# Optimization experiments

Hardware: AMD Instinct MI355X
Metric: run time of the kernel (lower is better)

The kernel has to match this reference:

```python
import jax, jax.numpy as jnp
import numpy as np

INPUT_SHIFT = 0.1
K = 3  # extract_image_patches(x, 3) hardcodes 3x3 patches


def extract_image_patches(x, k):
    # x: [B, C, H, W] -> [B, k*k*C, Ho, Wo], patch ordering (kh, kw, C)
    B, C, H, W = x.shape
    Ho, Wo = H - k + 1, W - k + 1
    slices = [x[:, :, i:i + Ho, j:j + Wo] for i in range(k) for j in range(k)]
    return jnp.concatenate(slices, axis=1)


def smooth_max(z, axis):
    # SMorph smooth maximum: sum(z * softmax(z)) along axis
    w = jax.nn.softmax(z, axis=axis)
    return jnp.sum(z * w, axis=axis)


def _branch(logp, kflat):
    # logp: [B, P, Ho, Wo]; kflat: [P, O] -> [B, O, Ho, Wo]
    z = logp[:, :, None] + kflat[None, :, :, None, None]  # [B, P, O, Ho, Wo]
    return jnp.exp(smooth_max(z, axis=1))


def setup_inputs() -> dict:
    key = jax.random.key(0)
    kx, kk1, kk2 = jax.random.split(key, 3)
    B, C, H, W, O = 4, 32, 32, 32, 64
    fan_in = K * K * C
    fan_out = K * K * O
    limit = float(np.sqrt(6.0 / (fan_in + fan_out)))  # xavier_uniform
    x = jax.random.normal(kx, (B, C, H, W), dtype=jnp.float32)
    k1 = jax.random.uniform(kk1, (K, K, C, O), minval=-limit, maxval=limit, dtype=jnp.float32)
    k2 = jax.random.uniform(kk2, (K, K, C, O), minval=-limit, maxval=limit, dtype=jnp.float32)
    bias = jnp.zeros((O,), dtype=jnp.float32)
    return {"x": x, "k1": k1, "k2": k2, "bias": bias}


def reference(x, k1, k2, bias):
    kh, kw, C, O = k1.shape
    k1f = k1.reshape(kh * kw * C, O)
    k2f = k2.reshape(kh * kw * C, O)
    # log of clamped patches for +x and -x
    p1 = jnp.log(jnp.maximum(extract_image_patches(x, K), INPUT_SHIFT))
    p2 = jnp.log(jnp.maximum(extract_image_patches(-x, K), INPUT_SHIFT))
    y11 = _branch(p1, k1f)
    y12 = _branch(p1, k2f)
    y21 = _branch(p2, k1f)
    y22 = _branch(p2, k2f)
    return y11 - y12 - y21 + y22 + bias[None, :, None, None]
```

## Files before the change

kernel.cpp:

```cpp
#include <hip/hip_runtime.h>
#include <math.h>


typedef float  f32x4 __attribute__((ext_vector_type(4)));
typedef short  s16x8 __attribute__((ext_vector_type(8)));

#define BB   4
#define CC   32
#define HH   32
#define WW   32
#define OO   64
#define HO   30
#define WO   30
#define NSP  900
#define KDIM 576

#define T1   131072
#define TB   18432

__device__ __forceinline__ unsigned short f2bf(float f) {
    unsigned u = __float_as_uint(f);
    return (unsigned short)((u + 0x7FFFu + ((u >> 16) & 1u)) >> 16);
}

__global__ __launch_bounds__(256) void smorph_prep(
    const float* __restrict__ x, const float* __restrict__ k1,
    const float* __restrict__ k2, float4* __restrict__ pixs,
    unsigned* __restrict__ pixm, unsigned short* __restrict__ bt)
{
    const int t = blockIdx.x * 256 + threadIdx.x;

    if (t < T1) {
        const int pix = t >> 5, c = t & 31;
        const int b = pix >> 10, h = (pix >> 5) & 31, w = pix & 31;
        float v = x[b*32768 + c*1024 + h*32 + w];
        float mp = fmaxf(v, 0.1f), mn = fmaxf(-v, 0.1f);
        float lp = mp * logf(mp), ln_ = mn * logf(mn);
        pixm[pix*64      + c] = (unsigned)f2bf(mp) | ((unsigned)f2bf(lp)  << 16);
        pixm[pix*64 + 32 + c] = (unsigned)f2bf(mn) | ((unsigned)f2bf(ln_) << 16);
        float s0 = mp, s1 = lp, s2 = mn, s3 = ln_;
#pragma unroll
        for (int m = 16; m >= 1; m >>= 1) {
            s0 += __shfl_xor(s0, m); s1 += __shfl_xor(s1, m);
            s2 += __shfl_xor(s2, m); s3 += __shfl_xor(s3, m);
        }
        if (c == 0) pixs[pix] = make_float4(s0, s1, s2, s3);
    } else if (t < T1 + TB) {
        const int u3 = t - T1;
        const int o = u3 & 63, p = u3 >> 6;
        const float a = k1[u3], b2 = k2[u3];
        const float d1 = expm1f(a),  q1 = a  * expf(a);
        const float d2 = expm1f(b2), q2 = b2 * expf(b2);
        const float vals[4][2] = {{d1, 0.f}, {q1, d1}, {d2, 0.f}, {q2, d2}};
#pragma unroll
        for (int tbl = 0; tbl < 4; ++tbl) {
            const int n = o*4 + tbl;
#pragma unroll
            for (int ks = 0; ks < 2; ++ks) {
                const int k    = 2*p + ks;
                const int st   = k >> 5, k32 = k & 31;
                const int lane = (n & 15) + ((k32 >> 3) << 4);
                bt[((n >> 4)*18 + st)*512 + lane*8 + (k32 & 7)] = f2bf(vals[tbl][ks]);
            }
        }
    }
}

__global__ __launch_bounds__(256, 2) void smorph_gemm(
    const unsigned* __restrict__ pixm, const unsigned short* __restrict__ bt,
    const float4* __restrict__ pixs, const float* __restrict__ bias,
    float* __restrict__ out)
{
    __shared__ float cmb[2][2048];
    __shared__ __align__(16) float epi[2][32*66];

    const int tid = threadIdx.x;
    const int l   = tid & 63;
    const int w   = tid >> 6;
    const int kq  = w >> 1;
    const int nhf = w & 1;
    const int bm  = blockIdx.x >> 1;
    const int nh  = blockIdx.x & 1;
    const int N0  = nh*128 + nhf*64;
    const int ng0 = N0 >> 4;

    const int lr = l & 15;
    const int lg = l >> 4;

    float4 S;
    {
        const int s  = bm*16 + lr;
        const int b  = s / NSP, r = s - b*NSP;
        const int ho = r / WO,  wo = r - WO*(r/WO);
        const float4* P = pixs + (b*1024 + ho*32 + wo);
        float4 a = make_float4(0,0,0,0);
#pragma unroll
        for (int kh = 0; kh < 3; ++kh)
#pragma unroll
            for (int kw = 0; kw < 3; ++kw) {
                float4 v = P[kh*32 + kw];
                a.x += v.x; a.y += v.y; a.z += v.z; a.w += v.w;
            }
        S = a;
    }

    unsigned offA[2];
    {
        const int sign = lr & 1;
#pragma unroll
        for (int mi = 0; mi < 2; ++mi) {
            const int s  = bm*16 + mi*8 + (lr >> 1);
            const int b  = s / NSP, r = s - b*NSP;
            const int ho = r / WO,  wo = r - WO*(r/WO);
            const int pix = b*1024 + ho*32 + wo;
            offA[mi] = (unsigned)(pix*256 + sign*128 + lg*16);
        }
    }

    const char* pa = (const char*)pixm;
    const char* pb = (const char*)bt;

    f32x4 acc[2][4] = {};

#pragma unroll
    for (int s2 = 0; s2 < 9; ++s2) {
        const int step  = s2*2 + kq;
        const int khkw  = step >> 1;
        const int kh    = khkw / 3, kw = khkw - 3*(khkw/3);
        const int khalf = step & 1;
        const unsigned immA = (unsigned)(kh*8192 + kw*256 + khalf*64);

        s16x8 a0 = *(const s16x8*)(pa + (offA[0] + immA));
        s16x8 a1 = *(const s16x8*)(pa + (offA[1] + immA));
        s16x8 b0 = *(const s16x8*)(pb + (((ng0+0)*18 + step)*64 + l)*16);
        s16x8 b1 = *(const s16x8*)(pb + (((ng0+1)*18 + step)*64 + l)*16);
        s16x8 b2 = *(const s16x8*)(pb + (((ng0+2)*18 + step)*64 + l)*16);
        s16x8 b3 = *(const s16x8*)(pb + (((ng0+3)*18 + step)*64 + l)*16);

        acc[0][0] = __builtin_amdgcn_mfma_f32_16x16x32_bf16(a0, b0, acc[0][0], 0, 0, 0);
        acc[0][1] = __builtin_amdgcn_mfma_f32_16x16x32_bf16(a0, b1, acc[0][1], 0, 0, 0);
        acc[0][2] = __builtin_amdgcn_mfma_f32_16x16x32_bf16(a0, b2, acc[0][2], 0, 0, 0);
        acc[0][3] = __builtin_amdgcn_mfma_f32_16x16x32_bf16(a0, b3, acc[0][3], 0, 0, 0);
        acc[1][0] = __builtin_amdgcn_mfma_f32_16x16x32_bf16(a1, b0, acc[1][0], 0, 0, 0);
        acc[1][1] = __builtin_amdgcn_mfma_f32_16x16x32_bf16(a1, b1, acc[1][1], 0, 0, 0);
        acc[1][2] = __builtin_amdgcn_mfma_f32_16x16x32_bf16(a1, b2, acc[1][2], 0, 0, 0);
        acc[1][3] = __builtin_amdgcn_mfma_f32_16x16x32_bf16(a1, b3, acc[1][3], 0, 0, 0);
    }

    if (kq == 1) {
#pragma unroll
        for (int mi = 0; mi < 2; ++mi)
#pragma unroll
            for (int ni = 0; ni < 4; ++ni)
#pragma unroll
                for (int r = 0; r < 4; ++r)
                    cmb[nhf][(mi*16 + ni*4 + r)*64 + l] = acc[mi][ni][r];
    }
    __syncthreads();
    if (kq == 0) {
#pragma unroll
        for (int mi = 0; mi < 2; ++mi)
#pragma unroll
            for (int ni = 0; ni < 4; ++ni)
#pragma unroll
                for (int r = 0; r < 4; ++r)
                    acc[mi][ni][r] += cmb[nhf][(mi*16 + ni*4 + r)*64 + l];

        const int wrbase = lg*4*66 + lr;
#pragma unroll
        for (int mi = 0; mi < 2; ++mi)
#pragma unroll
            for (int ni = 0; ni < 4; ++ni)
#pragma unroll
                for (int r = 0; r < 4; ++r)
                    epi[nhf][wrbase + (mi*16 + r)*66 + ni*16] = acc[mi][ni][r];
    }
    __syncthreads();

    if (kq == 0) {
        const int sl = lr;
        const int s  = bm*16 + sl;
        const int b  = s / NSP;
        const int r900 = s - b*NSP;
#pragma unroll
        for (int oi = 0; oi < 4; ++oi) {
            int ol = lg*4 + oi;
            int o  = (N0 >> 2) + ol;
            float4 v0 = *(const float4*)&epi[nhf][(2*sl + 0)*66 + ol*4];
            float4 v1 = *(const float4*)&epi[nhf][(2*sl + 1)*66 + ol*4];
            float d1p = S.x + v0.x, n1p = S.y + v0.y;
            float d2p = S.x + v0.z, n2p = S.y + v0.w;
            float d1n = S.z + v1.x, n1n = S.w + v1.y;
            float d2n = S.z + v1.z, n2n = S.w + v1.w;
            float P = __expf(n1p/d1p) - __expf(n2p/d2p)
                    - __expf(n1n/d1n) + __expf(n2n/d2n);
            out[((size_t)(b*OO + o))*NSP + r900] = P + bias[o];
        }
    }
}

extern "C" void kernel_launch(void* const* d_in, const int* in_sizes, int n_in,
                              void* d_out, int out_size, void* d_ws, size_t ws_size,
                              hipStream_t stream) {
    const float* x    = (const float*)d_in[0];
    const float* k1   = (const float*)d_in[1];
    const float* k2   = (const float*)d_in[2];
    const float* bias = (const float*)d_in[3];

    char* ws = (char*)d_ws;
    float4*         pixs = (float4*)(ws);
    unsigned*       pixm = (unsigned*)(ws + 0x10000);
    unsigned short* bt   = (unsigned short*)(ws + 0x110000);
    float*          out  = (float*)d_out;

    hipLaunchKernelGGL(smorph_prep, dim3((T1 + TB + 255)/256), dim3(256), 0, stream,
                       x, k1, k2, pixs, pixm, bt);
    hipLaunchKernelGGL(smorph_gemm, dim3(450), dim3(256), 0, stream,
                       pixm, bt, pixs, bias, out);
}
```

Baseline: 19.75 us.

## Split GEMM K-loop across four waves per N-half with tree reduction

```diff
diff --git a/kernel.cpp b/kernel.cpp
--- a/kernel.cpp
+++ b/kernel.cpp
@@ -66,12 +66,12 @@
     }
 }
 
-__global__ __launch_bounds__(256, 2) void smorph_gemm(
+__global__ __launch_bounds__(512, 2) void smorph_gemm(
     const unsigned* __restrict__ pixm, const unsigned short* __restrict__ bt,
     const float4* __restrict__ pixs, const float* __restrict__ bias,
     float* __restrict__ out)
 {
-    __shared__ float cmb[2][2048];
+    __shared__ float cmb[4][2048];
     __shared__ __align__(16) float epi[2][32*66];
 
     const int tid = threadIdx.x;
@@ -122,49 +122,75 @@
 
     f32x4 acc[2][4] = {};
 
-#pragma unroll
-    for (int s2 = 0; s2 < 9; ++s2) {
-        const int step  = s2*2 + kq;
-        const int khkw  = step >> 1;
-        const int kh    = khkw / 3, kw = khkw - 3*(khkw/3);
-        const int khalf = step & 1;
-        const unsigned immA = (unsigned)(kh*8192 + kw*256 + khalf*64);
-
-        s16x8 a0 = *(const s16x8*)(pa + (offA[0] + immA));
-        s16x8 a1 = *(const s16x8*)(pa + (offA[1] + immA));
-        s16x8 b0 = *(const s16x8*)(pb + (((ng0+0)*18 + step)*64 + l)*16);
-        s16x8 b1 = *(const s16x8*)(pb + (((ng0+1)*18 + step)*64 + l)*16);
-        s16x8 b2 = *(const s16x8*)(pb + (((ng0+2)*18 + step)*64 + l)*16);
-        s16x8 b3 = *(const s16x8*)(pb + (((ng0+3)*18 + step)*64 + l)*16);
-
-        acc[0][0] = __builtin_amdgcn_mfma_f32_16x16x32_bf16(a0, b0, acc[0][0], 0, 0, 0);
-        acc[0][1] = __builtin_amdgcn_mfma_f32_16x16x32_bf16(a0, b1, acc[0][1], 0, 0, 0);
-        acc[0][2] = __builtin_amdgcn_mfma_f32_16x16x32_bf16(a0, b2, acc[0][2], 0, 0, 0);
-        acc[0][3] = __builtin_amdgcn_mfma_f32_16x16x32_bf16(a0, b3, acc[0][3], 0, 0, 0);
-        acc[1][0] = __builtin_amdgcn_mfma_f32_16x16x32_bf16(a1, b0, acc[1][0], 0, 0, 0);
-        acc[1][1] = __builtin_amdgcn_mfma_f32_16x16x32_bf16(a1, b1, acc[1][1], 0, 0, 0);
-        acc[1][2] = __builtin_amdgcn_mfma_f32_16x16x32_bf16(a1, b2, acc[1][2], 0, 0, 0);
-        acc[1][3] = __builtin_amdgcn_mfma_f32_16x16x32_bf16(a1, b3, acc[1][3], 0, 0, 0);
-    }
-
+#define DO_STEP(stepv)                                                          \
+    {                                                                           \
+        const int step_ = (stepv);                                              \
+        const int khkw_ = step_ >> 1;                                           \
+        const int kh_   = khkw_ / 3, kw_ = khkw_ - 3*(khkw_/3);                 \
+        const unsigned immA_ = (unsigned)(kh_*8192 + kw_*256 + (step_ & 1)*64); \
+        s16x8 a0 = *(const s16x8*)(pa + (offA[0] + immA_));                     \
+        s16x8 a1 = *(const s16x8*)(pa + (offA[1] + immA_));                     \
+        s16x8 b0 = *(const s16x8*)(pb + (((ng0+0)*18 + step_)*64 + l)*16);      \
+        s16x8 b1 = *(const s16x8*)(pb + (((ng0+1)*18 + step_)*64 + l)*16);      \
+        s16x8 b2 = *(const s16x8*)(pb + (((ng0+2)*18 + step_)*64 + l)*16);      \
+        s16x8 b3 = *(const s16x8*)(pb + (((ng0+3)*18 + step_)*64 + l)*16);      \
+        acc[0][0] = __builtin_amdgcn_mfma_f32_16x16x32_bf16(a0, b0, acc[0][0], 0, 0, 0); \
+        acc[0][1] = __builtin_amdgcn_mfma_f32_16x16x32_bf16(a0, b1, acc[0][1], 0, 0, 0); \
+        acc[0][2] = __builtin_amdgcn_mfma_f32_16x16x32_bf16(a0, b2, acc[0][2], 0, 0, 0); \
+        acc[0][3] = __builtin_amdgcn_mfma_f32_16x16x32_bf16(a0, b3, acc[0][3], 0, 0, 0); \
+        acc[1][0] = __builtin_amdgcn_mfma_f32_16x16x32_bf16(a1, b0, acc[1][0], 0, 0, 0); \
+        acc[1][1] = __builtin_amdgcn_mfma_f32_16x16x32_bf16(a1, b1, acc[1][1], 0, 0, 0); \
+        acc[1][2] = __builtin_amdgcn_mfma_f32_16x16x32_bf16(a1, b2, acc[1][2], 0, 0, 0); \
+        acc[1][3] = __builtin_amdgcn_mfma_f32_16x16x32_bf16(a1, b3, acc[1][3], 0, 0, 0); \
+    }
+
+#pragma unroll
+    for (int s2 = 0; s2 < 4; ++s2) DO_STEP(s2*4 + kq);
+    if (kq < 2) DO_STEP(16 + kq);
+#undef DO_STEP
+
+    if (kq >= 2) {
+        float* dst = &cmb[(kq - 2)*2 + nhf][l];
+#pragma unroll
+        for (int mi = 0; mi < 2; ++mi)
+#pragma unroll
+            for (int ni = 0; ni < 4; ++ni)
+#pragma unroll
+                for (int r = 0; r < 4; ++r)
+                    dst[((mi*4 + ni)*4 + r)*64] = acc[mi][ni][r];
+    }
+    __syncthreads();
+    if (kq < 2) {
+        const float* srcp = &cmb[kq*2 + nhf][l];
+#pragma unroll
+        for (int mi = 0; mi < 2; ++mi)
+#pragma unroll
+            for (int ni = 0; ni < 4; ++ni)
+#pragma unroll
+                for (int r = 0; r < 4; ++r)
+                    acc[mi][ni][r] += srcp[((mi*4 + ni)*4 + r)*64];
+    }
+    __syncthreads();
     if (kq == 1) {
-#pragma unroll
-        for (int mi = 0; mi < 2; ++mi)
-#pragma unroll
-            for (int ni = 0; ni < 4; ++ni)
-#pragma unroll
-                for (int r = 0; r < 4; ++r)
-                    cmb[nhf][(mi*16 + ni*4 + r)*64 + l] = acc[mi][ni][r];
+        float* dst = &cmb[nhf][l];
+#pragma unroll
+        for (int mi = 0; mi < 2; ++mi)
+#pragma unroll
+            for (int ni = 0; ni < 4; ++ni)
+#pragma unroll
+                for (int r = 0; r < 4; ++r)
+                    dst[((mi*4 + ni)*4 + r)*64] = acc[mi][ni][r];
     }
     __syncthreads();
     if (kq == 0) {
-#pragma unroll
-        for (int mi = 0; mi < 2; ++mi)
-#pragma unroll
-            for (int ni = 0; ni < 4; ++ni)
-#pragma unroll
-                for (int r = 0; r < 4; ++r)
-                    acc[mi][ni][r] += cmb[nhf][(mi*16 + ni*4 + r)*64 + l];
+        const float* srcp = &cmb[nhf][l];
+#pragma unroll
+        for (int mi = 0; mi < 2; ++mi)
+#pragma unroll
+            for (int ni = 0; ni < 4; ++ni)
+#pragma unroll
+                for (int r = 0; r < 4; ++r)
+                    acc[mi][ni][r] += srcp[((mi*4 + ni)*4 + r)*64];
 
         const int wrbase = lg*4*66 + lr;
 #pragma unroll
@@ -215,6 +241,6 @@
 
     hipLaunchKernelGGL(smorph_prep, dim3((T1 + TB + 255)/256), dim3(256), 0, stream,
                        x, k1, k2, pixs, pixm, bt);
-    hipLaunchKernelGGL(smorph_gemm, dim3(450), dim3(256), 0, stream,
+    hipLaunchKernelGGL(smorph_gemm, dim3(450), dim3(512), 0, stream,
                        pixm, bt, pixs, bias, out);
 }
```

After: 20.60 us. +4.3%, slower.

## Double GEMM M-tile per block to reuse B fragments, halve grid

Applied to the files above, without the earlier changes.

```diff
diff --git a/kernel.cpp b/kernel.cpp
--- a/kernel.cpp
+++ b/kernel.cpp
@@ -13,6 +13,7 @@
 #define HO   30
 #define WO   30
 #define NSP  900
+#define MS   3600
 #define KDIM 576
 
 #define T1   131072
@@ -66,13 +67,14 @@
     }
 }
 
-__global__ __launch_bounds__(256, 2) void smorph_gemm(
+__global__ __launch_bounds__(256, 1) void smorph_gemm(
     const unsigned* __restrict__ pixm, const unsigned short* __restrict__ bt,
     const float4* __restrict__ pixs, const float* __restrict__ bias,
     float* __restrict__ out)
 {
-    __shared__ float cmb[2][2048];
-    __shared__ __align__(16) float epi[2][32*66];
+    __shared__ __align__(16) char ldsbuf[34816];
+    float* cmb = (float*)ldsbuf;
+    float* epi = (float*)ldsbuf;
 
     const int tid = threadIdx.x;
     const int l   = tid & 63;
@@ -87,29 +89,13 @@
     const int lr = l & 15;
     const int lg = l >> 4;
 
-    float4 S;
-    {
-        const int s  = bm*16 + lr;
-        const int b  = s / NSP, r = s - b*NSP;
-        const int ho = r / WO,  wo = r - WO*(r/WO);
-        const float4* P = pixs + (b*1024 + ho*32 + wo);
-        float4 a = make_float4(0,0,0,0);
-#pragma unroll
-        for (int kh = 0; kh < 3; ++kh)
-#pragma unroll
-            for (int kw = 0; kw < 3; ++kw) {
-                float4 v = P[kh*32 + kw];
-                a.x += v.x; a.y += v.y; a.z += v.z; a.w += v.w;
-            }
-        S = a;
-    }
-
-    unsigned offA[2];
+    unsigned offA[4];
     {
         const int sign = lr & 1;
 #pragma unroll
-        for (int mi = 0; mi < 2; ++mi) {
-            const int s  = bm*16 + mi*8 + (lr >> 1);
+        for (int mi = 0; mi < 4; ++mi) {
+            int s = bm*32 + mi*8 + (lr >> 1);
+            if (s > MS-1) s = MS-1;
             const int b  = s / NSP, r = s - b*NSP;
             const int ho = r / WO,  wo = r - WO*(r/WO);
             const int pix = b*1024 + ho*32 + wo;
@@ -120,18 +106,19 @@
     const char* pa = (const char*)pixm;
     const char* pb = (const char*)bt;
 
-    f32x4 acc[2][4] = {};
+    f32x4 acc[4][4] = {};
 
 #pragma unroll
     for (int s2 = 0; s2 < 9; ++s2) {
         const int step  = s2*2 + kq;
         const int khkw  = step >> 1;
         const int kh    = khkw / 3, kw = khkw - 3*(khkw/3);
-        const int khalf = step & 1;
-        const unsigned immA = (unsigned)(kh*8192 + kw*256 + khalf*64);
+        const unsigned immA = (unsigned)(kh*8192 + kw*256 + (step & 1)*64);
 
         s16x8 a0 = *(const s16x8*)(pa + (offA[0] + immA));
         s16x8 a1 = *(const s16x8*)(pa + (offA[1] + immA));
+        s16x8 a2 = *(const s16x8*)(pa + (offA[2] + immA));
+        s16x8 a3 = *(const s16x8*)(pa + (offA[3] + immA));
         s16x8 b0 = *(const s16x8*)(pb + (((ng0+0)*18 + step)*64 + l)*16);
         s16x8 b1 = *(const s16x8*)(pb + (((ng0+1)*18 + step)*64 + l)*16);
         s16x8 b2 = *(const s16x8*)(pb + (((ng0+2)*18 + step)*64 + l)*16);
@@ -145,56 +132,87 @@
         acc[1][1] = __builtin_amdgcn_mfma_f32_16x16x32_bf16(a1, b1, acc[1][1], 0, 0, 0);
         acc[1][2] = __builtin_amdgcn_mfma_f32_16x16x32_bf16(a1, b2, acc[1][2], 0, 0, 0);
         acc[1][3] = __builtin_amdgcn_mfma_f32_16x16x32_bf16(a1, b3, acc[1][3], 0, 0, 0);
+        acc[2][0] = __builtin_amdgcn_mfma_f32_16x16x32_bf16(a2, b0, acc[2][0], 0, 0, 0);
+        acc[2][1] = __builtin_amdgcn_mfma_f32_16x16x32_bf16(a2, b1, acc[2][1], 0, 0, 0);
+        acc[2][2] = __builtin_amdgcn_mfma_f32_16x16x32_bf16(a2, b2, acc[2][2], 0, 0, 0);
+        acc[2][3] = __builtin_amdgcn_mfma_f32_16x16x32_bf16(a2, b3, acc[2][3], 0, 0, 0);
+        acc[3][0] = __builtin_amdgcn_mfma_f32_16x16x32_bf16(a3, b0, acc[3][0], 0, 0, 0);
+        acc[3][1] = __builtin_amdgcn_mfma_f32_16x16x32_bf16(a3, b1, acc[3][1], 0, 0, 0);
+        acc[3][2] = __builtin_amdgcn_mfma_f32_16x16x32_bf16(a3, b2, acc[3][2], 0, 0, 0);
+        acc[3][3] = __builtin_amdgcn_mfma_f32_16x16x32_bf16(a3, b3, acc[3][3], 0, 0, 0);
     }
 
     if (kq == 1) {
-#pragma unroll
-        for (int mi = 0; mi < 2; ++mi)
+        float* dst = cmb + nhf*4096 + l;
+#pragma unroll
+        for (int mi = 0; mi < 4; ++mi)
 #pragma unroll
             for (int ni = 0; ni < 4; ++ni)
 #pragma unroll
                 for (int r = 0; r < 4; ++r)
-                    cmb[nhf][(mi*16 + ni*4 + r)*64 + l] = acc[mi][ni][r];
+                    dst[((mi*4 + ni)*4 + r)*64] = acc[mi][ni][r];
     }
     __syncthreads();
     if (kq == 0) {
-#pragma unroll
-        for (int mi = 0; mi < 2; ++mi)
+        const float* srcp = cmb + nhf*4096 + l;
+#pragma unroll
+        for (int mi = 0; mi < 4; ++mi)
 #pragma unroll
             for (int ni = 0; ni < 4; ++ni)
 #pragma unroll
                 for (int r = 0; r < 4; ++r)
-                    acc[mi][ni][r] += cmb[nhf][(mi*16 + ni*4 + r)*64 + l];
-
+                    acc[mi][ni][r] += srcp[((mi*4 + ni)*4 + r)*64];
+    }
+    __syncthreads();
+    if (kq == 0) {
+        float* E = epi + nhf*4224;
         const int wrbase = lg*4*66 + lr;
 #pragma unroll
-        for (int mi = 0; mi < 2; ++mi)
+        for (int mi = 0; mi < 4; ++mi)
 #pragma unroll
             for (int ni = 0; ni < 4; ++ni)
 #pragma unroll
                 for (int r = 0; r < 4; ++r)
-                    epi[nhf][wrbase + (mi*16 + r)*66 + ni*16] = acc[mi][ni][r];
+                    E[wrbase + (mi*16 + r)*66 + ni*16] = acc[mi][ni][r];
     }
     __syncthreads();
 
     if (kq == 0) {
-        const int sl = lr;
-        const int s  = bm*16 + sl;
-        const int b  = s / NSP;
-        const int r900 = s - b*NSP;
-#pragma unroll
-        for (int oi = 0; oi < 4; ++oi) {
-            int ol = lg*4 + oi;
-            int o  = (N0 >> 2) + ol;
-            float4 v0 = *(const float4*)&epi[nhf][(2*sl + 0)*66 + ol*4];
-            float4 v1 = *(const float4*)&epi[nhf][(2*sl + 1)*66 + ol*4];
-            float d1p = S.x + v0.x, n1p = S.y + v0.y;
-            float d2p = S.x + v0.z, n2p = S.y + v0.w;
-            float d1n = S.z + v1.x, n1n = S.w + v1.y;
-            float d2n = S.z + v1.z, n2n = S.w + v1.w;
-            float P = __expf(n1p/d1p) - __expf(n2p/d2p)
-                    - __expf(n1n/d1n) + __expf(n2n/d2n);
-            out[((size_t)(b*OO + o))*NSP + r900] = P + bias[o];
+        const float* E = epi + nhf*4224;
+#pragma unroll
+        for (int slh = 0; slh < 2; ++slh) {
+            const int sl = slh*16 + lr;
+            const int s  = bm*32 + sl;
+            const int sc = (s > MS-1) ? (MS-1) : s;
+            const int b  = sc / NSP, r900 = sc - b*NSP;
+            const int ho = r900 / WO, wo = r900 - WO*(r900/WO);
+
+            const float4* P = pixs + (b*1024 + ho*32 + wo);
+            float4 S = make_float4(0,0,0,0);
+#pragma unroll
+            for (int kh = 0; kh < 3; ++kh)
+#pragma unroll
+                for (int kw = 0; kw < 3; ++kw) {
+                    float4 v = P[kh*32 + kw];
+                    S.x += v.x; S.y += v.y; S.z += v.z; S.w += v.w;
+                }
+
+            if (s < MS) {
+#pragma unroll
+                for (int oi = 0; oi < 4; ++oi) {
+                    int ol = lg*4 + oi;
+                    int o  = (N0 >> 2) + ol;
+                    float4 v0 = *(const float4*)&E[(2*sl + 0)*66 + ol*4];
+                    float4 v1 = *(const float4*)&E[(2*sl + 1)*66 + ol*4];
+                    float d1p = S.x + v0.x, n1p = S.y + v0.y;
+                    float d2p = S.x + v0.z, n2p = S.y + v0.w;
+                    float d1n = S.z + v1.x, n1n = S.w + v1.y;
+                    float d2n = S.z + v1.z, n2n = S.w + v1.w;
+                    float Pv = __expf(n1p/d1p) - __expf(n2p/d2p)
+                             - __expf(n1n/d1n) + __expf(n2n/d2n);
+                    out[((size_t)(b*OO + o))*NSP + r900] = Pv + bias[o];
+                }
+            }
         }
     }
 }
@@ -215,6 +233,6 @@
 
     hipLaunchKernelGGL(smorph_prep, dim3((T1 + TB + 255)/256), dim3(256), 0, stream,
                        x, k1, k2, pixs, pixm, bt);
-    hipLaunchKernelGGL(smorph_gemm, dim3(450), dim3(256), 0, stream,
+    hipLaunchKernelGGL(smorph_gemm, dim3(226), dim3(256), 0, stream,
                        pixm, bt, pixs, bias, out);
 }
```

Result: slower. 21.10 us (+6.8%).
